# Kernel tuning notes

Measured on AMD Instinct MI355X. Metric: run time of the kernel, lower is better.

Reference implementation:

```python
import jax, jax.numpy as jnp
import numpy as np

DROPOUT_P = 0.5  # pre-softmax dropout prob from __init__
_MASK_KEY = jax.random.key(42)  # fixed key -> deterministic dropout mask


def setup_inputs() -> dict:
    key = jax.random.key(0)
    kq, kk, kv = jax.random.split(key, 3)
    shape = (4, 16, 1024, 64)  # [B, H, S, D]
    Q = jax.random.normal(kq, shape, dtype=jnp.float32)
    K = jax.random.normal(kk, shape, dtype=jnp.float32)
    V = jax.random.normal(kv, shape, dtype=jnp.float32)
    return {"Q": Q, "K": K, "V": V}


def reference(Q, K, V):
    # scores: [B, H, S, S] = Q @ K^T  (no 1/sqrt(d) scaling: scale=False)
    scores = jnp.einsum("bhqd,bhkd->bhqk", Q, K)
    # pre-softmax dropout (train mode, p=0.5), deterministic fixed-key mask
    keep = jax.random.bernoulli(_MASK_KEY, 1.0 - DROPOUT_P, scores.shape)
    scores = jnp.where(keep, scores / (1.0 - DROPOUT_P), 0.0)
    attn = jax.nn.softmax(scores, axis=-1)
    return jnp.einsum("bhqk,bhkd->bhqd", attn, V)
```

## Files before the change

### kernel.cpp

```cpp
#include <hip/hip_runtime.h>
#include <hip/hip_bf16.h>
#include <hip/hip_fp16.h>
#include <math.h>

typedef _Float16 f16x8 __attribute__((ext_vector_type(8)));
typedef __fp16  h16x2 __attribute__((ext_vector_type(2)));
typedef float f32x4 __attribute__((ext_vector_type(4)));

#define S_LEN 1024
#define DH 64
#define KVB 64
#define NIT 16
#define KROW 72
#define THR 11.0f

__device__ __forceinline__ unsigned rotl(unsigned x, unsigned r) {
  return __builtin_amdgcn_alignbit(x, x, 32u - r);
}

__device__ __forceinline__ bool keep_bit(unsigned e) {
  const unsigned ks1 = 42u;
  const unsigned ks2 = 0x1BD11BF0u;
  unsigned x0 = 0u;
  unsigned x1 = e + ks1;
#define TFR(Ra,Rb,Rc,Rd) \
  x0 += x1; x1 = rotl(x1, Ra); x1 ^= x0; \
  x0 += x1; x1 = rotl(x1, Rb); x1 ^= x0; \
  x0 += x1; x1 = rotl(x1, Rc); x1 ^= x0; \
  x0 += x1; x1 = rotl(x1, Rd); x1 ^= x0;
  TFR(13u,15u,26u, 6u)  x0 += ks1; x1 += ks2 + 1u;
  TFR(17u,29u,16u,24u)  x0 += ks2; x1 += 2u;
  TFR(13u,15u,26u, 6u)     x1 += ks1 + 3u;
  TFR(17u,29u,16u,24u)  x0 += ks1; x1 += ks2 + 4u;
  TFR(13u,15u,26u, 6u)  x0 += ks2; x1 += 5u;
#undef TFR
  return ((x0 ^ x1) >> 31) == 0u;
}

__device__ __forceinline__ f16x8 pk8(f32x4 a, f32x4 b) {
  h16x2 p0 = __builtin_amdgcn_cvt_pkrtz(a[0], a[1]);
  h16x2 p1 = __builtin_amdgcn_cvt_pkrtz(a[2], a[3]);
  h16x2 p2 = __builtin_amdgcn_cvt_pkrtz(b[0], b[1]);
  h16x2 p3 = __builtin_amdgcn_cvt_pkrtz(b[2], b[3]);
  f16x8 r;
  r[0]=(_Float16)p0[0]; r[1]=(_Float16)p0[1]; r[2]=(_Float16)p1[0]; r[3]=(_Float16)p1[1];
  r[4]=(_Float16)p2[0]; r[5]=(_Float16)p2[1]; r[6]=(_Float16)p3[0]; r[7]=(_Float16)p3[1];
  return r;
}

__global__ __launch_bounds__(256)
void attn_dropout_kernel(const float* __restrict__ Q, const float* __restrict__ K,
                         const float* __restrict__ V, float* __restrict__ out) {
  __shared__ _Float16 Kl[KVB][KROW];
  __shared__ _Float16 Pl[4][16][KROW];

  const unsigned bh   = blockIdx.x >> 4;
  const unsigned q0   = (blockIdx.x & 15u) * 64u;
  const unsigned tid  = threadIdx.x;
  const unsigned w    = tid >> 6;
  const unsigned lane = tid & 63u;
  const unsigned g    = lane >> 4;
  const unsigned ln   = lane & 15u;
  const unsigned qw   = q0 + w * 16u;

  f16x8 Qa0, Qa1;
  {
    const float* Qp = Q + (size_t)(bh * S_LEN + qw + ln) * DH + g * 8;
    const float s = 2.885390082f;
    f32x4 a = *(const f32x4*)(Qp)      * s;
    f32x4 b = *(const f32x4*)(Qp + 4)  * s;
    f32x4 c = *(const f32x4*)(Qp + 32) * s;
    f32x4 d = *(const f32x4*)(Qp + 36) * s;
    Qa0 = pk8(a, b);
    Qa1 = pk8(c, d);
  }

  float mrun[4], lpart[4];
  f32x4 accO[4];
#pragma unroll
  for (int r = 0; r < 4; ++r) { mrun[r] = -1e30f; lpart[r] = 0.0f; }
#pragma unroll
  for (int n = 0; n < 4; ++n) accO[n] = (f32x4){0.f, 0.f, 0.f, 0.f};

  const unsigned kk  = tid >> 2;
  const unsigned dgf = (tid & 3u) * 16u;

  f32x4 kr0, kr1, kr2, kr3;
  {
    const float* Kp = K + (size_t)(bh * S_LEN + kk) * DH + dgf;
    kr0 = *(const f32x4*)(Kp);  kr1 = *(const f32x4*)(Kp + 4);
    kr2 = *(const f32x4*)(Kp + 8); kr3 = *(const f32x4*)(Kp + 12);
  }

  const float* Vg_base = V + (size_t)bh * S_LEN * DH + g * 8 * DH + ln;

  for (int t = 0; t < NIT; ++t) {
    __syncthreads();
    *(f16x8*)&Kl[kk][dgf]     = pk8(kr0, kr1);
    *(f16x8*)&Kl[kk][dgf + 8] = pk8(kr2, kr3);
    __syncthreads();

    {
      int tn = (t + 1 < NIT) ? t + 1 : NIT - 1;
      const float* Kp = K + (size_t)(bh * S_LEN + tn * KVB + kk) * DH + dgf;
      kr0 = *(const f32x4*)(Kp);  kr1 = *(const f32x4*)(Kp + 4);
      kr2 = *(const f32x4*)(Kp + 8); kr3 = *(const f32x4*)(Kp + 12);
    }

    f16x8 vb0[4], vb1[4];
    {
      const float* Vg = Vg_base + (size_t)t * KVB * DH;
#pragma unroll
      for (int nd = 0; nd < 4; ++nd) {
        f32x4 a, b, c, d;
#pragma unroll
        for (int j = 0; j < 4; ++j) {
          a[j] = Vg[(j)      * DH + nd * 16];
          b[j] = Vg[(4 + j)  * DH + nd * 16];
          c[j] = Vg[(32 + j) * DH + nd * 16];
          d[j] = Vg[(36 + j) * DH + nd * 16];
        }
        vb0[nd] = pk8(a, b);
        vb1[nd] = pk8(c, d);
      }
    }

    f32x4 sc[4];
#pragma unroll
    for (int nt = 0; nt < 4; ++nt) {
      f16x8 kb0 = *(const f16x8*)&Kl[nt * 16 + ln][g * 8];
      f16x8 kb1 = *(const f16x8*)&Kl[nt * 16 + ln][32 + g * 8];
      f32x4 a = (f32x4){0.f, 0.f, 0.f, 0.f};
      a = __builtin_amdgcn_mfma_f32_16x16x32_f16(Qa0, kb0, a, 0, 0, 0);
      a = __builtin_amdgcn_mfma_f32_16x16x32_f16(Qa1, kb1, a, 0, 0, 0);
      sc[nt] = a;
    }

    float sm[4][4];
    float pmx[4];
#pragma unroll
    for (int r = 0; r < 4; ++r) pmx[r] = -1e30f;
#pragma unroll
    for (int nt = 0; nt < 4; ++nt) {
#pragma unroll
      for (int r = 0; r < 4; ++r) {
        unsigned q  = qw + g * 4 + r;
        unsigned kg = (unsigned)t * KVB + nt * 16 + ln;
        unsigned e  = (bh << 20) + (q << 10) + kg;
        float v = keep_bit(e) ? sc[nt][r] : 0.0f;
        sm[nt][r] = v;
        pmx[r] = fmaxf(pmx[r], v);
      }
    }

    bool need = (pmx[0] > mrun[0] + THR) | (pmx[1] > mrun[1] + THR) |
                (pmx[2] > mrun[2] + THR) | (pmx[3] > mrun[3] + THR);
    if (__any(need)) {
#pragma unroll
      for (int r = 0; r < 4; ++r) {
        float mx = pmx[r];
#pragma unroll
        for (int off = 1; off < 16; off <<= 1) mx = fmaxf(mx, __shfl_xor(mx, off));
        float mn  = fmaxf(mrun[r], mx);
        float scl = exp2f(mrun[r] - mn);
        mrun[r] = mn;
        lpart[r] *= scl;
#pragma unroll
        for (int n = 0; n < 4; ++n) accO[n][r] *= scl;
      }
    }

    float ps[4][4];
#pragma unroll
    for (int nt = 0; nt < 4; ++nt) {
#pragma unroll
      for (int r = 0; r < 4; ++r) {
        float p = exp2f(sm[nt][r] - mrun[r]);
        ps[nt][r] = p;
        lpart[r] += p;
      }
    }

#pragma unroll
    for (int nt = 0; nt < 4; ++nt)
#pragma unroll
      for (int r = 0; r < 4; ++r)
        Pl[w][g * 4 + r][nt * 16 + ln] = (_Float16)ps[nt][r];

    f16x8 Pa0 = *(const f16x8*)&Pl[w][ln][g * 8];
    f16x8 Pa1 = *(const f16x8*)&Pl[w][ln][32 + g * 8];
#pragma unroll
    for (int nd = 0; nd < 4; ++nd) {
      accO[nd] = __builtin_amdgcn_mfma_f32_16x16x32_f16(Pa0, vb0[nd], accO[nd], 0, 0, 0);
      accO[nd] = __builtin_amdgcn_mfma_f32_16x16x32_f16(Pa1, vb1[nd], accO[nd], 0, 0, 0);
    }
  }

  float lf[4];
#pragma unroll
  for (int r = 0; r < 4; ++r) {
    float l = lpart[r];
#pragma unroll
    for (int off = 1; off < 16; off <<= 1) l += __shfl_xor(l, off);
    lf[r] = l;
  }
#pragma unroll
  for (int nd = 0; nd < 4; ++nd) {
#pragma unroll
    for (int r = 0; r < 4; ++r) {
      unsigned q = qw + g * 4 + r;
      out[(size_t)(bh * S_LEN + q) * DH + nd * 16 + ln] = accO[nd][r] / lf[r];
    }
  }
}

extern "C" void kernel_launch(void* const* d_in, const int* in_sizes, int n_in,
                              void* d_out, int out_size, void* d_ws, size_t ws_size,
                              hipStream_t stream) {
  const float* Q = (const float*)d_in[0];
  const float* K = (const float*)d_in[1];
  const float* V = (const float*)d_in[2];
  float* out = (float*)d_out;
  dim3 grid(64 * 16);
  dim3 block(256);
  hipLaunchKernelGGL(attn_dropout_kernel, grid, block, 0, stream, Q, K, V, out);
}
```

Measured before the change: 251.3 us.

## Load K directly from global per wave, drop shared-memory K staging and barriers

```diff
diff --git a/kernel.cpp b/kernel.cpp
--- a/kernel.cpp
+++ b/kernel.cpp
@@ -11,7 +11,7 @@
 #define DH 64
 #define KVB 64
 #define NIT 16
-#define KROW 72
+#define PROW 68
 #define THR 11.0f
 
 __device__ __forceinline__ unsigned rotl(unsigned x, unsigned r) {
@@ -51,8 +51,7 @@
 __global__ __launch_bounds__(256)
 void attn_dropout_kernel(const float* __restrict__ Q, const float* __restrict__ K,
                          const float* __restrict__ V, float* __restrict__ out) {
-  __shared__ _Float16 Kl[KVB][KROW];
-  __shared__ _Float16 Pl[4][16][KROW];
+  __shared__ _Float16 Pl[4][16][PROW];
 
   const unsigned bh   = blockIdx.x >> 4;
   const unsigned q0   = (blockIdx.x & 15u) * 64u;
@@ -82,58 +81,27 @@
 #pragma unroll
   for (int n = 0; n < 4; ++n) accO[n] = (f32x4){0.f, 0.f, 0.f, 0.f};
 
-  const unsigned kk  = tid >> 2;
-  const unsigned dgf = (tid & 3u) * 16u;
-
-  f32x4 kr0, kr1, kr2, kr3;
-  {
-    const float* Kp = K + (size_t)(bh * S_LEN + kk) * DH + dgf;
-    kr0 = *(const f32x4*)(Kp);  kr1 = *(const f32x4*)(Kp + 4);
-    kr2 = *(const f32x4*)(Kp + 8); kr3 = *(const f32x4*)(Kp + 12);
-  }
-
-  const float* Vg_base = V + (size_t)bh * S_LEN * DH + g * 8 * DH + ln;
+  const float* Kb = K + ((size_t)bh * S_LEN + ln) * DH + g * 8;
+  const float* Vb = V + ((size_t)bh * S_LEN + g * 8) * DH + ln;
 
   for (int t = 0; t < NIT; ++t) {
-    __syncthreads();
-    *(f16x8*)&Kl[kk][dgf]     = pk8(kr0, kr1);
-    *(f16x8*)&Kl[kk][dgf + 8] = pk8(kr2, kr3);
-    __syncthreads();
-
+    f32x4 sc[4];
     {
-      int tn = (t + 1 < NIT) ? t + 1 : NIT - 1;
-      const float* Kp = K + (size_t)(bh * S_LEN + tn * KVB + kk) * DH + dgf;
-      kr0 = *(const f32x4*)(Kp);  kr1 = *(const f32x4*)(Kp + 4);
-      kr2 = *(const f32x4*)(Kp + 8); kr3 = *(const f32x4*)(Kp + 12);
-    }
-
-    f16x8 vb0[4], vb1[4];
-    {
-      const float* Vg = Vg_base + (size_t)t * KVB * DH;
-#pragma unroll
-      for (int nd = 0; nd < 4; ++nd) {
-        f32x4 a, b, c, d;
-#pragma unroll
-        for (int j = 0; j < 4; ++j) {
-          a[j] = Vg[(j)      * DH + nd * 16];
-          b[j] = Vg[(4 + j)  * DH + nd * 16];
-          c[j] = Vg[(32 + j) * DH + nd * 16];
-          d[j] = Vg[(36 + j) * DH + nd * 16];
-        }
-        vb0[nd] = pk8(a, b);
-        vb1[nd] = pk8(c, d);
-      }
-    }
-
-    f32x4 sc[4];
-#pragma unroll
-    for (int nt = 0; nt < 4; ++nt) {
-      f16x8 kb0 = *(const f16x8*)&Kl[nt * 16 + ln][g * 8];
-      f16x8 kb1 = *(const f16x8*)&Kl[nt * 16 + ln][32 + g * 8];
-      f32x4 a = (f32x4){0.f, 0.f, 0.f, 0.f};
-      a = __builtin_amdgcn_mfma_f32_16x16x32_f16(Qa0, kb0, a, 0, 0, 0);
-      a = __builtin_amdgcn_mfma_f32_16x16x32_f16(Qa1, kb1, a, 0, 0, 0);
-      sc[nt] = a;
+      const float* Kt = Kb + (size_t)t * KVB * DH;
+#pragma unroll
+      for (int nt = 0; nt < 4; ++nt) {
+        const float* Kp = Kt + nt * 16 * DH;
+        f32x4 a = *(const f32x4*)(Kp);
+        f32x4 b = *(const f32x4*)(Kp + 4);
+        f32x4 c = *(const f32x4*)(Kp + 32);
+        f32x4 d = *(const f32x4*)(Kp + 36);
+        f16x8 kb0 = pk8(a, b);
+        f16x8 kb1 = pk8(c, d);
+        f32x4 acc = (f32x4){0.f, 0.f, 0.f, 0.f};
+        acc = __builtin_amdgcn_mfma_f32_16x16x32_f16(Qa0, kb0, acc, 0, 0, 0);
+        acc = __builtin_amdgcn_mfma_f32_16x16x32_f16(Qa1, kb1, acc, 0, 0, 0);
+        sc[nt] = acc;
+      }
     }
 
     float sm[4][4];
@@ -170,29 +138,39 @@
       }
     }
 
-    float ps[4][4];
+    f32x4 va[4], vbx[4], vc[4], vd[4];
+    {
+      const float* Vt = Vb + (size_t)t * KVB * DH;
+#pragma unroll
+      for (int nd = 0; nd < 4; ++nd) {
+#pragma unroll
+        for (int j = 0; j < 4; ++j) {
+          va[nd][j]  = Vt[(j)      * DH + nd * 16];
+          vbx[nd][j] = Vt[(4 + j)  * DH + nd * 16];
+          vc[nd][j]  = Vt[(32 + j) * DH + nd * 16];
+          vd[nd][j]  = Vt[(36 + j) * DH + nd * 16];
+        }
+      }
+    }
+
 #pragma unroll
     for (int nt = 0; nt < 4; ++nt) {
 #pragma unroll
       for (int r = 0; r < 4; ++r) {
         float p = exp2f(sm[nt][r] - mrun[r]);
-        ps[nt][r] = p;
         lpart[r] += p;
-      }
-    }
-
-#pragma unroll
-    for (int nt = 0; nt < 4; ++nt)
-#pragma unroll
-      for (int r = 0; r < 4; ++r)
-        Pl[w][g * 4 + r][nt * 16 + ln] = (_Float16)ps[nt][r];
+        Pl[w][g * 4 + r][nt * 16 + ln] = (_Float16)p;
+      }
+    }
 
     f16x8 Pa0 = *(const f16x8*)&Pl[w][ln][g * 8];
     f16x8 Pa1 = *(const f16x8*)&Pl[w][ln][32 + g * 8];
 #pragma unroll
     for (int nd = 0; nd < 4; ++nd) {
-      accO[nd] = __builtin_amdgcn_mfma_f32_16x16x32_f16(Pa0, vb0[nd], accO[nd], 0, 0, 0);
-      accO[nd] = __builtin_amdgcn_mfma_f32_16x16x32_f16(Pa1, vb1[nd], accO[nd], 0, 0, 0);
+      f16x8 v0 = pk8(va[nd], vbx[nd]);
+      f16x8 v1 = pk8(vc[nd], vd[nd]);
+      accO[nd] = __builtin_amdgcn_mfma_f32_16x16x32_f16(Pa0, v0, accO[nd], 0, 0, 0);
+      accO[nd] = __builtin_amdgcn_mfma_f32_16x16x32_f16(Pa1, v1, accO[nd], 0, 0, 0);
     }
   }
 
```

After: 256.5 us. 2.0% more time.
